# Kernel optimization log

Hardware: AMD Instinct MI355X
Metric: run time of the kernel (lower is better)

## Reference

```python
import jax, jax.numpy as jnp
import numpy as np

D = 512
H = 8
DK = D // H
FF = 4 * D
EPS = 1e-5
NEG = -1.0e9


def _layernorm(x, g, b):
    mu = jnp.mean(x, axis=-1, keepdims=True)
    var = jnp.mean((x - mu) ** 2, axis=-1, keepdims=True)
    return (x - mu) * jax.lax.rsqrt(var + EPS) * g + b


def setup_inputs() -> dict:
    key = jax.random.key(0)
    ks = jax.random.split(key, 16)
    B, S = 4, 2048
    x = jax.random.normal(ks[0], (B, S, D), dtype=jnp.float32)
    # causal mask, broadcastable to [B, H, S, S]; mask==0 -> blocked
    mask = jnp.tril(jnp.ones((S, S), dtype=jnp.int32))[None, None]
    s = 1.0 / np.sqrt(D)
    sf = 1.0 / np.sqrt(FF)
    p = {
        "wq": jax.random.normal(ks[1], (D, D), jnp.float32) * s,
        "bq": jnp.zeros((D,), jnp.float32),
        "wk": jax.random.normal(ks[2], (D, D), jnp.float32) * s,
        "bk": jnp.zeros((D,), jnp.float32),
        "wv": jax.random.normal(ks[3], (D, D), jnp.float32) * s,
        "bv": jnp.zeros((D,), jnp.float32),
        "wo": jax.random.normal(ks[4], (D, D), jnp.float32) * s,
        "bo": jnp.zeros((D,), jnp.float32),
        "w1": jax.random.normal(ks[5], (D, FF), jnp.float32) * s,
        "b1": jnp.zeros((FF,), jnp.float32),
        "w2": jax.random.normal(ks[6], (FF, D), jnp.float32) * sf,
        "b2": jnp.zeros((D,), jnp.float32),
        "g1": jnp.ones((D,), jnp.float32),
        "be1": jnp.zeros((D,), jnp.float32),
        "g2": jnp.ones((D,), jnp.float32),
        "be2": jnp.zeros((D,), jnp.float32),
    }
    return {"x": x, "mask": mask, **p}


def reference(x, mask, wq, bq, wk, bk, wv, bv, wo, bo, w1, b1, w2, b2, g1, be1, g2, be2):
    B, S, _ = x.shape
    # projections -> [B, H, S, DK]
    q = (x @ wq + bq).reshape(B, S, H, DK).transpose(0, 2, 1, 3)
    k = (x @ wk + bk).reshape(B, S, H, DK).transpose(0, 2, 1, 3)
    v = (x @ wv + bv).reshape(B, S, H, DK).transpose(0, 2, 1, 3)
    scores = jnp.einsum("bhqd,bhkd->bhqk", q, k) / np.sqrt(DK)
    scores = jnp.where(mask == 0, NEG, scores)
    attn = jax.nn.softmax(scores, axis=-1)
    ctx = jnp.einsum("bhqk,bhkd->bhqd", attn, v)
    ctx = ctx.transpose(0, 2, 1, 3).reshape(B, S, D)
    attn_out = ctx @ wo + bo
    # dropout is inference-mode identity
    h = _layernorm(x + attn_out, g1, be1)
    ffn = jax.nn.relu(h @ w1 + b1) @ w2 + b2
    return _layernorm(h + ffn, g2, be2)
```

## Files before the change

### kernel.cpp

```cpp
#include <hip/hip_runtime.h>
#include <math.h>

#define D_   512
#define H_   8
#define DK_  64
#define FF_  2048
#define S_   2048
#define B_   4
#define M_   (B_*S_)
#define EPS_ 1e-5f
#define SCLQ 0.1803368801111f

typedef __attribute__((ext_vector_type(8))) short bf16x8;
typedef __attribute__((ext_vector_type(4))) float f32x4;

__device__ inline unsigned short f2b(float f) {
    unsigned u = __builtin_bit_cast(unsigned, f);
    unsigned r = (u + 0x7FFFu + ((u >> 16) & 1u)) >> 16;
    return (unsigned short)r;
}
__device__ inline unsigned short f2b_trunc(float f) {
    return (unsigned short)(__builtin_bit_cast(unsigned, f) >> 16);
}
__device__ inline float b2f(unsigned short u) {
    return __builtin_bit_cast(float, (unsigned)u << 16);
}

__device__ __forceinline__ void async_cp16(const void* g, void* l) {
    __builtin_amdgcn_global_load_lds(
        (const __attribute__((address_space(1))) unsigned int*)g,
        (__attribute__((address_space(3))) unsigned int*)l, 16, 0, 0);
}

__global__ __launch_bounds__(256)
void prep_kernel(const float* __restrict__ x,
                 const float* __restrict__ wq, const float* __restrict__ wk,
                 const float* __restrict__ wv, const float* __restrict__ wo,
                 const float* __restrict__ bq, const float* __restrict__ bk,
                 const float* __restrict__ bv,
                 const float* __restrict__ w1, const float* __restrict__ w2,
                 unsigned short* __restrict__ xb, unsigned short* __restrict__ wqkvt,
                 unsigned short* __restrict__ wot, unsigned short* __restrict__ w1t,
                 unsigned short* __restrict__ w2t, float* __restrict__ bqkv)
{
    __shared__ float L[32][33];
    const int bid = blockIdx.x;
    const int tid = threadIdx.x;

    if (bid < 2048) {
        const int i = (bid * 256 + tid) * 8;
        const float4 a = *(const float4*)(x + i);
        const float4 b = *(const float4*)(x + i + 4);
        bf16x8 v;
        v[0] = (short)f2b(a.x); v[1] = (short)f2b(a.y);
        v[2] = (short)f2b(a.z); v[3] = (short)f2b(a.w);
        v[4] = (short)f2b(b.x); v[5] = (short)f2b(b.y);
        v[6] = (short)f2b(b.z); v[7] = (short)f2b(b.w);
        *(bf16x8*)(xb + i) = v;
        return;
    }

    const float* w; unsigned short* wt; int K, N, k0, n0; float scl = 1.f;
    if (bid < 3072) {
        const int z = (bid - 2048) >> 8;
        const int r = (bid - 2048) & 255;
        n0 = (r & 15) * 32; k0 = (r >> 4) * 32; K = 512; N = 512;
        w  = (z == 0) ? wq : (z == 1) ? wk : (z == 2) ? wv : wo;
        wt = (z < 3) ? (wqkvt + (size_t)z * 512 * 512) : wot;
        if (z == 0) scl = SCLQ;
        if (z < 3 && r == 0) {
            const float* bsrc = (z == 0) ? bq : (z == 1) ? bk : bv;
            const float bscl  = (z == 0) ? SCLQ : 1.f;
            bqkv[z * 512 + tid]       = bsrc[tid] * bscl;
            bqkv[z * 512 + 256 + tid] = bsrc[256 + tid] * bscl;
        }
    } else if (bid < 4096) {
        const int r = bid - 3072;
        n0 = (r & 63) * 32; k0 = (r >> 6) * 32; K = 512; N = 2048;
        w = w1; wt = w1t;
    } else {
        const int r = bid - 4096;
        n0 = (r & 15) * 32; k0 = (r >> 4) * 32; K = 2048; N = 512;
        w = w2; wt = w2t;
    }

    const int xx = tid & 31, y = tid >> 5;
#pragma unroll
    for (int i = 0; i < 4; i++)
        L[y + i * 8][xx] = w[(size_t)(k0 + y + i * 8) * N + n0 + xx] * scl;
    __syncthreads();
#pragma unroll
    for (int i = 0; i < 4; i++)
        wt[(size_t)(n0 + y + i * 8) * K + k0 + xx] = f2b(L[xx][y + i * 8]);
}

template<int WR, int WC, int MT, int NT, int OUTB, int RELU, int RESADD, int HASBIAS>
__global__ __launch_bounds__(256)
void gemm_bf16(const unsigned short* __restrict__ A, const unsigned short* __restrict__ Bt,
               const float* __restrict__ bias, const void* __restrict__ RES,
               void* __restrict__ Cv, int K, int lda, int ldb, int ldc)
{
    constexpr int BM = WR * MT * 16;
    constexpr int BN = WC * NT * 16;
    constexpr int CA = BM / 64;
    constexpr int CB = BN / 64;
    __shared__ unsigned short As[2][BM * 32];
    __shared__ unsigned short Bs[2][BN * 32];

    const int tid  = threadIdx.x;
    const int lane = tid & 63;
    const int w    = tid >> 6;
    const int wr   = w / WC, wc = w % WC;
    const int quad = lane >> 4;
    const int l15  = lane & 15;
    const int n0   = blockIdx.x * BN;
    const int m0   = blockIdx.y * BM;

    f32x4 acc[MT][NT];
#pragma unroll
    for (int i = 0; i < MT; i++)
#pragma unroll
        for (int j = 0; j < NT; j++) acc[i][j] = (f32x4){0.f, 0.f, 0.f, 0.f};

    auto stage = [&](int k0, int bufi) {
#pragma unroll
        for (int i = 0; i < CA; i++) {
            const int c = tid + i * 256;
            async_cp16(&A[(size_t)(m0 + (c >> 2)) * lda + k0 + (c & 3) * 8], &As[bufi][c * 8]);
        }
#pragma unroll
        for (int i = 0; i < CB; i++) {
            const int c = tid + i * 256;
            async_cp16(&Bt[(size_t)(n0 + (c >> 2)) * ldb + k0 + (c & 3) * 8], &Bs[bufi][c * 8]);
        }
    };

    stage(0, 0);
    const int niter = K >> 5;
    for (int ii = 0; ii < niter; ii++) {
        const int knext = (ii + 1 < niter) ? (ii + 1) * 32 : 0;
        stage(knext, (ii + 1) & 1);
        __builtin_amdgcn_s_waitcnt(0x0f70 | (CA + CB));
        __builtin_amdgcn_s_barrier();

        const unsigned short* Ac = &As[ii & 1][0];
        const unsigned short* Bc = &Bs[ii & 1][0];
        bf16x8 af[MT], bfr[NT];
#pragma unroll
        for (int t = 0; t < MT; t++)
            af[t]  = *(const bf16x8*)&Ac[(wr * MT * 16 + t * 16 + l15) * 32 + quad * 8];
#pragma unroll
        for (int t = 0; t < NT; t++)
            bfr[t] = *(const bf16x8*)&Bc[(wc * NT * 16 + t * 16 + l15) * 32 + quad * 8];
#pragma unroll
        for (int mt = 0; mt < MT; mt++)
#pragma unroll
            for (int nt = 0; nt < NT; nt++)
                acc[mt][nt] = __builtin_amdgcn_mfma_f32_16x16x32_bf16(
                    af[mt], bfr[nt], acc[mt][nt], 0, 0, 0);
        __builtin_amdgcn_s_barrier();
    }

#pragma unroll
    for (int mt = 0; mt < MT; mt++) {
        const int rowb = m0 + wr * MT * 16 + mt * 16 + quad * 4;
#pragma unroll
        for (int nt = 0; nt < NT; nt++) {
            const int col = n0 + wc * NT * 16 + nt * 16 + l15;
            const float bv = HASBIAS ? bias[col] : 0.f;
#pragma unroll
            for (int r = 0; r < 4; r++) {
                const size_t idx = (size_t)(rowb + r) * ldc + col;
                float v = acc[mt][nt][r] + bv;
                if (RESADD == 1) v += ((const float*)RES)[idx];
                if (RESADD == 2) v += b2f(((const unsigned short*)RES)[idx]);
                if (RELU)   v = fmaxf(v, 0.f);
                if (OUTB) ((unsigned short*)Cv)[idx] = f2b(v);
                else      ((float*)Cv)[idx] = v;
            }
        }
    }
}

__global__ __launch_bounds__(256)
void vtrans(const unsigned short* __restrict__ qkv, unsigned short* __restrict__ vt)
{
    __shared__ unsigned short L[64][72];
    const int s0 = blockIdx.x * 64;
    const int bh = blockIdx.y;
    const int b  = bh >> 3, hh = bh & 7;
    const int tid = threadIdx.x;
    const unsigned short* src = qkv + (size_t)(b * S_) * 1536 + 1024 + hh * 64;
#pragma unroll
    for (int i = 0; i < 2; i++) {
        const int c = tid + i * 256;
        const int r = c >> 3, sub = (c & 7) * 8;
        *(bf16x8*)&L[r][sub] = *(const bf16x8*)(src + (size_t)(s0 + r) * 1536 + sub);
    }
    __syncthreads();
    const int dk = tid >> 2;
    const int sc = (tid & 3) * 16;
    bf16x8 t0, t1;
#pragma unroll
    for (int j = 0; j < 8; j++) t0[j] = (short)L[sc + j][dk];
#pragma unroll
    for (int j = 0; j < 8; j++) t1[j] = (short)L[sc + 8 + j][dk];
    unsigned short* dst = vt + (size_t)(bh * 64 + dk) * S_ + s0 + sc;
    *(bf16x8*)(dst)     = t0;
    *(bf16x8*)(dst + 8) = t1;
}

__global__ __launch_bounds__(256)
void attn_mfma(const unsigned short* __restrict__ qkv,
               const unsigned short* __restrict__ vt,
               unsigned short* __restrict__ ctx)
{
    constexpr int LDP = 72;
    __shared__ unsigned short Ks[2][64 * 64];
    __shared__ unsigned short Vs[2][64 * 64];
    __shared__ unsigned short Ps[4][16 * LDP];

    const int tid  = threadIdx.x;
    const int lane = tid & 63;
    const int w    = tid >> 6;
    const int quad = lane >> 4;
    const int l15  = lane & 15;
    const int pi   = blockIdx.x >> 5;
    const int bh   = blockIdx.x & 31;
    const int b    = bh >> 3, hh = bh & 7;

    const unsigned short* qbase = qkv + (size_t)(b * S_) * 1536 + hh * 64;
    const unsigned short* kbase = qbase + 512;
    const unsigned short* vtb   = vt + (size_t)bh * 64 * S_;
    unsigned short* pw = &Ps[w][0];

    bf16x8 ones;
#pragma unroll
    for (int j = 0; j < 8; j++) ones[j] = (short)0x3F80;

    auto stage = [&](int kb, int bufi) {
        unsigned short* kd = &Ks[bufi][0];
        unsigned short* vd = &Vs[bufi][0];
#pragma unroll
        for (int i = 0; i < 2; i++) {
            const int c = tid + i * 256;
            const int row = c >> 3;
            const int l = (c & 7) ^ (row & 7);
            async_cp16(kbase + (size_t)(kb * 64 + row) * 1536 + l * 8, kd + c * 8);
            async_cp16(vtb + (size_t)row * S_ + kb * 64 + l * 8, vd + c * 8);
        }
    };

    stage(0, 0);
    int it = 0;
    const int kc_d = (w >> 1) + 1;
    const int rhs_mask = w * 16 + quad * 4;

    for (int phase = 0; phase < 2; phase++) {
        const int qb    = phase ? pi : (31 - pi);
        const int qrow0 = qb * 64 + w * 16;

        bf16x8 qf[2];
        {
            const unsigned short* qr = qbase + (size_t)(qrow0 + l15) * 1536;
            qf[0] = *(const bf16x8*)(qr + quad * 8);
            qf[1] = *(const bf16x8*)(qr + 32 + quad * 8);
        }

        f32x4 Oacc[5];
#pragma unroll
        for (int i = 0; i < 5; i++) Oacc[i] = (f32x4){0.f, 0.f, 0.f, 0.f};

        for (int kb = 0; kb < qb; kb++) {
            stage(kb + 1, (it + 1) & 1);
            __builtin_amdgcn_s_waitcnt(0x0F74);
            __builtin_amdgcn_s_barrier();
            const unsigned short* Kc = &Ks[it & 1][0];
            const unsigned short* Vc = &Vs[it & 1][0];

            f32x4 sacc[4];
#pragma unroll
            for (int nt = 0; nt < 4; nt++) sacc[nt] = (f32x4){0.f, 0.f, 0.f, 0.f};
#pragma unroll
            for (int kc = 0; kc < 2; kc++)
#pragma unroll
                for (int nt = 0; nt < 4; nt++) {
                    const int phys = (kc * 4 + quad) ^ (l15 & 7);
                    const bf16x8 kf = *(const bf16x8*)&Kc[(nt * 16 + l15) * 64 + phys * 8];
                    sacc[nt] = __builtin_amdgcn_mfma_f32_16x16x32_bf16(qf[kc], kf, sacc[nt], 0, 0, 0);
                }
#pragma unroll
            for (int r = 0; r < 4; r++)
#pragma unroll
                for (int nt = 0; nt < 4; nt++)
                    pw[(quad * 4 + r) * LDP + nt * 16 + l15] = f2b_trunc(exp2f(sacc[nt][r]));
#pragma unroll
            for (int kc = 0; kc < 2; kc++) {
                const bf16x8 af = *(const bf16x8*)&pw[l15 * LDP + kc * 32 + quad * 8];
#pragma unroll
                for (int nt = 0; nt < 4; nt++) {
                    const int phys = (kc * 4 + quad) ^ (l15 & 7);
                    const bf16x8 vf = *(const bf16x8*)&Vc[(nt * 16 + l15) * 64 + phys * 8];
                    Oacc[nt] = __builtin_amdgcn_mfma_f32_16x16x32_bf16(af, vf, Oacc[nt], 0, 0, 0);
                }
                Oacc[4] = __builtin_amdgcn_mfma_f32_16x16x32_bf16(af, ones, Oacc[4], 0, 0, 0);
            }
            __builtin_amdgcn_s_barrier();
            it++;
        }

        {
            stage(0, (it + 1) & 1);
            __builtin_amdgcn_s_waitcnt(0x0F74);
            __builtin_amdgcn_s_barrier();
            const unsigned short* Kc = &Ks[it & 1][0];
            const unsigned short* Vc = &Vs[it & 1][0];

            f32x4 sacc[4];
#pragma unroll
            for (int nt = 0; nt < 4; nt++) sacc[nt] = (f32x4){0.f, 0.f, 0.f, 0.f};
#pragma unroll
            for (int kc = 0; kc < 2; kc++)
#pragma unroll
                for (int nt = 0; nt < 4; nt++) {
                    if (nt > w) continue;
                    const int phys = (kc * 4 + quad) ^ (l15 & 7);
                    const bf16x8 kf = *(const bf16x8*)&Kc[(nt * 16 + l15) * 64 + phys * 8];
                    sacc[nt] = __builtin_amdgcn_mfma_f32_16x16x32_bf16(qf[kc], kf, sacc[nt], 0, 0, 0);
                }
#pragma unroll
            for (int r = 0; r < 4; r++) {
                const int rhs = rhs_mask + r;
#pragma unroll
                for (int nt = 0; nt < 4; nt++) {
                    float s = sacc[nt][r];
                    if (nt * 16 + l15 > rhs) s = -1.0e9f;
                    pw[(quad * 4 + r) * LDP + nt * 16 + l15] = f2b_trunc(exp2f(s));
                }
            }
#pragma unroll
            for (int kc = 0; kc < 2; kc++) {
                if (kc < kc_d) {
                    const bf16x8 af = *(const bf16x8*)&pw[l15 * LDP + kc * 32 + quad * 8];
#pragma unroll
                    for (int nt = 0; nt < 4; nt++) {
                        const int phys = (kc * 4 + quad) ^ (l15 & 7);
                        const bf16x8 vf = *(const bf16x8*)&Vc[(nt * 16 + l15) * 64 + phys * 8];
                        Oacc[nt] = __builtin_amdgcn_mfma_f32_16x16x32_bf16(af, vf, Oacc[nt], 0, 0, 0);
                    }
                    Oacc[4] = __builtin_amdgcn_mfma_f32_16x16x32_bf16(af, ones, Oacc[4], 0, 0, 0);
                }
            }
            __builtin_amdgcn_s_barrier();
            it++;
        }

        const int orow = qrow0 + quad * 4;
        unsigned short* cb = ctx + (size_t)(b * S_) * 512 + hh * 64;
#pragma unroll
        for (int r = 0; r < 4; r++) {
            const float lsum = __shfl(Oacc[4][r], (lane & 48));
            const float inv = 1.f / lsum;
#pragma unroll
            for (int nt = 0; nt < 4; nt++)
                cb[(size_t)(orow + r) * 512 + nt * 16 + l15] = f2b(Oacc[nt][r] * inv);
        }
    }
}

template<int WF, int WB>
__global__ __launch_bounds__(256)
void ln_kernel(const float* __restrict__ s, const float* __restrict__ g,
               const float* __restrict__ be, float* __restrict__ out,
               unsigned short* __restrict__ outb)
{
    const int wave = threadIdx.x >> 6;
    const int lane = threadIdx.x & 63;
    const int row  = blockIdx.x * 4 + wave;
    const float* ps = s + (size_t)row * D_;
    const int c0 = lane * 4;

    float v[8];
    {
        const float4 a0 = *(const float4*)(ps + c0);
        const float4 a1 = *(const float4*)(ps + c0 + 256);
        v[0] = a0.x; v[1] = a0.y; v[2] = a0.z; v[3] = a0.w;
        v[4] = a1.x; v[5] = a1.y; v[6] = a1.z; v[7] = a1.w;
    }

    float sum = 0.f;
#pragma unroll
    for (int i = 0; i < 8; i++) sum += v[i];
#pragma unroll
    for (int m = 1; m < 64; m <<= 1) sum += __shfl_xor(sum, m);
    const float mu = sum * (1.f / D_);

    float sq = 0.f;
#pragma unroll
    for (int i = 0; i < 8; i++) { const float d = v[i] - mu; sq += d * d; }
#pragma unroll
    for (int m = 1; m < 64; m <<= 1) sq += __shfl_xor(sq, m);
    const float rstd = rsqrtf(sq * (1.f / D_) + EPS_);

    const float4 g0 = *(const float4*)(g + c0);
    const float4 b0 = *(const float4*)(be + c0);
    const float4 g1 = *(const float4*)(g + c0 + 256);
    const float4 b1 = *(const float4*)(be + c0 + 256);

    float o[8];
    o[0] = (v[0] - mu) * rstd * g0.x + b0.x;
    o[1] = (v[1] - mu) * rstd * g0.y + b0.y;
    o[2] = (v[2] - mu) * rstd * g0.z + b0.z;
    o[3] = (v[3] - mu) * rstd * g0.w + b0.w;
    o[4] = (v[4] - mu) * rstd * g1.x + b1.x;
    o[5] = (v[5] - mu) * rstd * g1.y + b1.y;
    o[6] = (v[6] - mu) * rstd * g1.z + b1.z;
    o[7] = (v[7] - mu) * rstd * g1.w + b1.w;

    if (WF) {
        *(float4*)(out + (size_t)row * D_ + c0)       = *(float4*)&o[0];
        *(float4*)(out + (size_t)row * D_ + c0 + 256) = *(float4*)&o[4];
    }
    if (WB) {
        short4 vb0 = (short4){(short)f2b(o[0]), (short)f2b(o[1]), (short)f2b(o[2]), (short)f2b(o[3])};
        short4 vb1 = (short4){(short)f2b(o[4]), (short)f2b(o[5]), (short)f2b(o[6]), (short)f2b(o[7])};
        *(short4*)(outb + (size_t)row * D_ + c0)       = vb0;
        *(short4*)(outb + (size_t)row * D_ + c0 + 256) = vb1;
    }
}

extern "C" void kernel_launch(void* const* d_in, const int* in_sizes, int n_in,
                              void* d_out, int out_size, void* d_ws, size_t ws_size,
                              hipStream_t stream)
{
    const float* x  = (const float*)d_in[0];
    const float* wq = (const float*)d_in[2];
    const float* bq = (const float*)d_in[3];
    const float* wk = (const float*)d_in[4];
    const float* bk = (const float*)d_in[5];
    const float* wv = (const float*)d_in[6];
    const float* bv = (const float*)d_in[7];
    const float* wo = (const float*)d_in[8];
    const float* bo = (const float*)d_in[9];
    const float* w1 = (const float*)d_in[10];
    const float* b1 = (const float*)d_in[11];
    const float* w2 = (const float*)d_in[12];
    const float* b2 = (const float*)d_in[13];
    const float* g1 = (const float*)d_in[14];
    const float* be1= (const float*)d_in[15];
    const float* g2 = (const float*)d_in[16];
    const float* be2= (const float*)d_in[17];
    float* out = (float*)d_out;

    const size_t MB = 1048576;
    char* w8 = (char*)d_ws;
    unsigned short* wqkvt = (unsigned short*)(w8 + 0);
    unsigned short* wot   = (unsigned short*)(w8 + 1572864);
    unsigned short* w1t   = (unsigned short*)(w8 + 2097152);
    unsigned short* w2t   = (unsigned short*)(w8 + 4194304);
    float*          bqkv  = (float*)(w8 + 6291456);
    unsigned short* qkv   = (unsigned short*)(w8 + 8 * MB);
    unsigned short* ffn1b = qkv;
    unsigned short* xb    = (unsigned short*)(w8 + 40 * MB);
    unsigned short* ctx   = xb;
    unsigned short* vt    = (unsigned short*)(w8 + 48 * MB);
    unsigned short* hb    = vt;
    float*          pre   = (float*)(w8 + 56 * MB);

    const dim3 blk(256);

    prep_kernel<<<dim3(5120), blk, 0, stream>>>(
        x, wq, wk, wv, wo, bq, bk, bv, w1, w2, xb, wqkvt, wot, w1t, w2t, bqkv);

    gemm_bf16<2,2,4,4,1,0,0,1><<<dim3(12, 64), blk, 0, stream>>>(
        xb, wqkvt, bqkv, nullptr, qkv, 512, 512, 512, 1536);

    vtrans<<<dim3(32, 32), blk, 0, stream>>>(qkv, vt);

    attn_mfma<<<dim3(512), blk, 0, stream>>>(qkv, vt, ctx);

    gemm_bf16<2,2,2,4,0,0,1,1><<<dim3(4, 128), blk, 0, stream>>>(
        ctx, wot, bo, x, pre, 512, 512, 512, 512);

    ln_kernel<0,1><<<dim3(M_ / 4), blk, 0, stream>>>(pre, g1, be1, nullptr, hb);

    gemm_bf16<2,2,4,4,1,1,0,1><<<dim3(16, 64), blk, 0, stream>>>(
        hb, w1t, b1, nullptr, ffn1b, 512, 512, 512, 2048);

    gemm_bf16<2,2,2,4,0,0,2,1><<<dim3(4, 128), blk, 0, stream>>>(
        ffn1b, w2t, b2, hb, pre, 2048, 2048, 2048, 512);

    ln_kernel<1,0><<<dim3(M_ / 4), blk, 0, stream>>>(pre, g2, be2, out, nullptr);
}
```

Before: 286.1 us.

## Keep attention probabilities in registers and split causal pairs into separate blocks

The attention kernel now computes S transposed (K as the A operand), packs exp2 probabilities to bf16 in registers and redistributes them with cross-lane shuffles into the PV operand layout. This replaces the per-wave LDS round trip for P. It also drops the paired heavy/light q-block scheme: each of 1024 blocks handles a single q-block, with launch bounds requesting 4 blocks per CU. The goal is less LDS traffic and more parallelism. The cost is extra shuffle instructions and load imbalance that now depends on scheduling order, with heavy blocks dispatched first.

```diff
diff --git a/kernel.cpp b/kernel.cpp
--- a/kernel.cpp
+++ b/kernel.cpp
@@ -13,17 +13,19 @@
 
 typedef __attribute__((ext_vector_type(8))) short bf16x8;
 typedef __attribute__((ext_vector_type(4))) float f32x4;
+typedef __attribute__((ext_vector_type(4))) unsigned int u32x4;
 
 __device__ inline unsigned short f2b(float f) {
     unsigned u = __builtin_bit_cast(unsigned, f);
     unsigned r = (u + 0x7FFFu + ((u >> 16) & 1u)) >> 16;
     return (unsigned short)r;
 }
-__device__ inline unsigned short f2b_trunc(float f) {
-    return (unsigned short)(__builtin_bit_cast(unsigned, f) >> 16);
-}
 __device__ inline float b2f(unsigned short u) {
     return __builtin_bit_cast(float, (unsigned)u << 16);
+}
+__device__ inline unsigned packbf(float p0, float p1) {
+    return (__builtin_bit_cast(unsigned, p1) & 0xFFFF0000u) |
+           (__builtin_bit_cast(unsigned, p0) >> 16);
 }
 
 __device__ __forceinline__ void async_cp16(const void* g, void* l) {
@@ -210,29 +212,31 @@
     *(bf16x8*)(dst + 8) = t1;
 }
 
-__global__ __launch_bounds__(256)
+__global__ __launch_bounds__(256, 4)
 void attn_mfma(const unsigned short* __restrict__ qkv,
                const unsigned short* __restrict__ vt,
                unsigned short* __restrict__ ctx)
 {
-    constexpr int LDP = 72;
     __shared__ unsigned short Ks[2][64 * 64];
     __shared__ unsigned short Vs[2][64 * 64];
-    __shared__ unsigned short Ps[4][16 * LDP];
 
     const int tid  = threadIdx.x;
     const int lane = tid & 63;
     const int w    = tid >> 6;
     const int quad = lane >> 4;
     const int l15  = lane & 15;
-    const int pi   = blockIdx.x >> 5;
-    const int bh   = blockIdx.x & 31;
+    const int bid  = blockIdx.x;
+    const int qb   = 31 - (bid >> 5);
+    const int bh   = bid & 31;
     const int b    = bh >> 3, hh = bh & 7;
 
     const unsigned short* qbase = qkv + (size_t)(b * S_) * 1536 + hh * 64;
     const unsigned short* kbase = qbase + 512;
     const unsigned short* vtb   = vt + (size_t)bh * 64 * S_;
-    unsigned short* pw = &Ps[w][0];
+
+    const int srcA  = 32 * (quad & 1) + l15;
+    const int srcB  = srcA + 16;
+    const bool selHi = (quad >> 1) != 0;
 
     bf16x8 ones;
 #pragma unroll
@@ -251,120 +255,128 @@
         }
     };
 
+    const int qrow0 = qb * 64 + w * 16;
+    bf16x8 qf[2];
+    {
+        const unsigned short* qr = qbase + (size_t)(qrow0 + l15) * 1536;
+        qf[0] = *(const bf16x8*)(qr + quad * 8);
+        qf[1] = *(const bf16x8*)(qr + 32 + quad * 8);
+    }
+
+    f32x4 Oacc[5];
+#pragma unroll
+    for (int i = 0; i < 5; i++) Oacc[i] = (f32x4){0.f, 0.f, 0.f, 0.f};
+
     stage(0, 0);
-    int it = 0;
-    const int kc_d = (w >> 1) + 1;
-    const int rhs_mask = w * 16 + quad * 4;
-
-    for (int phase = 0; phase < 2; phase++) {
-        const int qb    = phase ? pi : (31 - pi);
-        const int qrow0 = qb * 64 + w * 16;
-
-        bf16x8 qf[2];
-        {
-            const unsigned short* qr = qbase + (size_t)(qrow0 + l15) * 1536;
-            qf[0] = *(const bf16x8*)(qr + quad * 8);
-            qf[1] = *(const bf16x8*)(qr + 32 + quad * 8);
-        }
-
-        f32x4 Oacc[5];
-#pragma unroll
-        for (int i = 0; i < 5; i++) Oacc[i] = (f32x4){0.f, 0.f, 0.f, 0.f};
-
-        for (int kb = 0; kb < qb; kb++) {
-            stage(kb + 1, (it + 1) & 1);
-            __builtin_amdgcn_s_waitcnt(0x0F74);
-            __builtin_amdgcn_s_barrier();
-            const unsigned short* Kc = &Ks[it & 1][0];
-            const unsigned short* Vc = &Vs[it & 1][0];
-
-            f32x4 sacc[4];
-#pragma unroll
-            for (int nt = 0; nt < 4; nt++) sacc[nt] = (f32x4){0.f, 0.f, 0.f, 0.f};
-#pragma unroll
-            for (int kc = 0; kc < 2; kc++)
-#pragma unroll
-                for (int nt = 0; nt < 4; nt++) {
-                    const int phys = (kc * 4 + quad) ^ (l15 & 7);
-                    const bf16x8 kf = *(const bf16x8*)&Kc[(nt * 16 + l15) * 64 + phys * 8];
-                    sacc[nt] = __builtin_amdgcn_mfma_f32_16x16x32_bf16(qf[kc], kf, sacc[nt], 0, 0, 0);
-                }
-#pragma unroll
-            for (int r = 0; r < 4; r++)
-#pragma unroll
-                for (int nt = 0; nt < 4; nt++)
-                    pw[(quad * 4 + r) * LDP + nt * 16 + l15] = f2b_trunc(exp2f(sacc[nt][r]));
-#pragma unroll
-            for (int kc = 0; kc < 2; kc++) {
-                const bf16x8 af = *(const bf16x8*)&pw[l15 * LDP + kc * 32 + quad * 8];
-#pragma unroll
-                for (int nt = 0; nt < 4; nt++) {
-                    const int phys = (kc * 4 + quad) ^ (l15 & 7);
-                    const bf16x8 vf = *(const bf16x8*)&Vc[(nt * 16 + l15) * 64 + phys * 8];
-                    Oacc[nt] = __builtin_amdgcn_mfma_f32_16x16x32_bf16(af, vf, Oacc[nt], 0, 0, 0);
-                }
-                Oacc[4] = __builtin_amdgcn_mfma_f32_16x16x32_bf16(af, ones, Oacc[4], 0, 0, 0);
+
+    auto pv_chunk = [&](const unsigned pk[4][2], int kc, const unsigned short* Vc) {
+        const unsigned tA0 = __shfl(pk[kc * 2][0],     srcA, 64);
+        const unsigned tA1 = __shfl(pk[kc * 2][1],     srcA, 64);
+        const unsigned tB0 = __shfl(pk[kc * 2 + 1][0], srcA, 64);
+        const unsigned tB1 = __shfl(pk[kc * 2 + 1][1], srcA, 64);
+        const unsigned uA0 = __shfl(pk[kc * 2][0],     srcB, 64);
+        const unsigned uA1 = __shfl(pk[kc * 2][1],     srcB, 64);
+        const unsigned uB0 = __shfl(pk[kc * 2 + 1][0], srcB, 64);
+        const unsigned uB1 = __shfl(pk[kc * 2 + 1][1], srcB, 64);
+        u32x4 a;
+        a[0] = selHi ? tB0 : tA0;
+        a[1] = selHi ? tB1 : tA1;
+        a[2] = selHi ? uB0 : uA0;
+        a[3] = selHi ? uB1 : uA1;
+        const bf16x8 af = __builtin_bit_cast(bf16x8, a);
+#pragma unroll
+        for (int nt = 0; nt < 4; nt++) {
+            const int phys = (kc * 4 + quad) ^ (l15 & 7);
+            const bf16x8 vf = *(const bf16x8*)&Vc[(nt * 16 + l15) * 64 + phys * 8];
+            Oacc[nt] = __builtin_amdgcn_mfma_f32_16x16x32_bf16(af, vf, Oacc[nt], 0, 0, 0);
+        }
+        Oacc[4] = __builtin_amdgcn_mfma_f32_16x16x32_bf16(af, ones, Oacc[4], 0, 0, 0);
+    };
+
+    for (int kb = 0; kb < qb; kb++) {
+        stage(kb + 1, (kb + 1) & 1);
+        __builtin_amdgcn_s_waitcnt(0x0F74);
+        __builtin_amdgcn_s_barrier();
+        const unsigned short* Kc = &Ks[kb & 1][0];
+        const unsigned short* Vc = &Vs[kb & 1][0];
+
+        f32x4 st[4];
+#pragma unroll
+        for (int nt = 0; nt < 4; nt++) st[nt] = (f32x4){0.f, 0.f, 0.f, 0.f};
+#pragma unroll
+        for (int kc = 0; kc < 2; kc++)
+#pragma unroll
+            for (int nt = 0; nt < 4; nt++) {
+                const int phys = (kc * 4 + quad) ^ (l15 & 7);
+                const bf16x8 kf = *(const bf16x8*)&Kc[(nt * 16 + l15) * 64 + phys * 8];
+                st[nt] = __builtin_amdgcn_mfma_f32_16x16x32_bf16(kf, qf[kc], st[nt], 0, 0, 0);
             }
-            __builtin_amdgcn_s_barrier();
-            it++;
-        }
-
-        {
-            stage(0, (it + 1) & 1);
-            __builtin_amdgcn_s_waitcnt(0x0F74);
-            __builtin_amdgcn_s_barrier();
-            const unsigned short* Kc = &Ks[it & 1][0];
-            const unsigned short* Vc = &Vs[it & 1][0];
-
-            f32x4 sacc[4];
-#pragma unroll
-            for (int nt = 0; nt < 4; nt++) sacc[nt] = (f32x4){0.f, 0.f, 0.f, 0.f};
-#pragma unroll
-            for (int kc = 0; kc < 2; kc++)
-#pragma unroll
-                for (int nt = 0; nt < 4; nt++) {
-                    if (nt > w) continue;
-                    const int phys = (kc * 4 + quad) ^ (l15 & 7);
-                    const bf16x8 kf = *(const bf16x8*)&Kc[(nt * 16 + l15) * 64 + phys * 8];
-                    sacc[nt] = __builtin_amdgcn_mfma_f32_16x16x32_bf16(qf[kc], kf, sacc[nt], 0, 0, 0);
-                }
+
+        unsigned pk[4][2];
+#pragma unroll
+        for (int nt = 0; nt < 4; nt++) {
+            const float p0 = exp2f(st[nt][0]);
+            const float p1 = exp2f(st[nt][1]);
+            const float p2 = exp2f(st[nt][2]);
+            const float p3 = exp2f(st[nt][3]);
+            pk[nt][0] = packbf(p0, p1);
+            pk[nt][1] = packbf(p2, p3);
+        }
+
+        pv_chunk(pk, 0, Vc);
+        pv_chunk(pk, 1, Vc);
+        __builtin_amdgcn_s_barrier();
+    }
+
+    {
+        stage(0, (qb + 1) & 1);
+        __builtin_amdgcn_s_waitcnt(0x0F74);
+        __builtin_amdgcn_s_barrier();
+        const unsigned short* Kc = &Ks[qb & 1][0];
+        const unsigned short* Vc = &Vs[qb & 1][0];
+
+        f32x4 st[4];
+#pragma unroll
+        for (int nt = 0; nt < 4; nt++) st[nt] = (f32x4){0.f, 0.f, 0.f, 0.f};
+#pragma unroll
+        for (int kc = 0; kc < 2; kc++)
+#pragma unroll
+            for (int nt = 0; nt < 4; nt++) {
+                if (nt > w) continue;
+                const int phys = (kc * 4 + quad) ^ (l15 & 7);
+                const bf16x8 kf = *(const bf16x8*)&Kc[(nt * 16 + l15) * 64 + phys * 8];
+                st[nt] = __builtin_amdgcn_mfma_f32_16x16x32_bf16(kf, qf[kc], st[nt], 0, 0, 0);
+            }
+
+        const int rhs = w * 16 + l15;
+        unsigned pk[4][2];
+#pragma unroll
+        for (int nt = 0; nt < 4; nt++) {
+            const int kb0 = nt * 16 + quad * 4;
+            float p[4];
 #pragma unroll
             for (int r = 0; r < 4; r++) {
-                const int rhs = rhs_mask + r;
-#pragma unroll
-                for (int nt = 0; nt < 4; nt++) {
-                    float s = sacc[nt][r];
-                    if (nt * 16 + l15 > rhs) s = -1.0e9f;
-                    pw[(quad * 4 + r) * LDP + nt * 16 + l15] = f2b_trunc(exp2f(s));
-                }
+                float s = st[nt][r];
+                if (kb0 + r > rhs) s = -1.0e9f;
+                p[r] = exp2f(s);
             }
-#pragma unroll
-            for (int kc = 0; kc < 2; kc++) {
-                if (kc < kc_d) {
-                    const bf16x8 af = *(const bf16x8*)&pw[l15 * LDP + kc * 32 + quad * 8];
-#pragma unroll
-                    for (int nt = 0; nt < 4; nt++) {
-                        const int phys = (kc * 4 + quad) ^ (l15 & 7);
-                        const bf16x8 vf = *(const bf16x8*)&Vc[(nt * 16 + l15) * 64 + phys * 8];
-                        Oacc[nt] = __builtin_amdgcn_mfma_f32_16x16x32_bf16(af, vf, Oacc[nt], 0, 0, 0);
-                    }
-                    Oacc[4] = __builtin_amdgcn_mfma_f32_16x16x32_bf16(af, ones, Oacc[4], 0, 0, 0);
-                }
-            }
-            __builtin_amdgcn_s_barrier();
-            it++;
-        }
-
-        const int orow = qrow0 + quad * 4;
-        unsigned short* cb = ctx + (size_t)(b * S_) * 512 + hh * 64;
-#pragma unroll
-        for (int r = 0; r < 4; r++) {
-            const float lsum = __shfl(Oacc[4][r], (lane & 48));
-            const float inv = 1.f / lsum;
-#pragma unroll
-            for (int nt = 0; nt < 4; nt++)
-                cb[(size_t)(orow + r) * 512 + nt * 16 + l15] = f2b(Oacc[nt][r] * inv);
-        }
+            pk[nt][0] = packbf(p[0], p[1]);
+            pk[nt][1] = packbf(p[2], p[3]);
+        }
+
+        const int kc_d = (w >> 1) + 1;
+        pv_chunk(pk, 0, Vc);
+        if (kc_d > 1) pv_chunk(pk, 1, Vc);
+    }
+
+    const int orow = qrow0 + quad * 4;
+    unsigned short* cb = ctx + (size_t)(b * S_) * 512 + hh * 64;
+#pragma unroll
+    for (int r = 0; r < 4; r++) {
+        const float inv = 1.f / Oacc[4][r];
+#pragma unroll
+        for (int nt = 0; nt < 4; nt++)
+            cb[(size_t)(orow + r) * 512 + nt * 16 + l15] = f2b(Oacc[nt][r] * inv);
     }
 }
 
@@ -477,7 +489,7 @@
 
     vtrans<<<dim3(32, 32), blk, 0, stream>>>(qkv, vt);
 
-    attn_mfma<<<dim3(512), blk, 0, stream>>>(qkv, vt, ctx);
+    attn_mfma<<<dim3(1024), blk, 0, stream>>>(qkv, vt, ctx);
 
     gemm_bf16<2,2,2,4,0,0,1,1><<<dim3(4, 128), blk, 0, stream>>>(
         ctx, wot, bo, x, pre, 512, 512, 512, 512);
```

Result: no change. 289.7 us (+1.3%).
